# Performance work log

Measured on AMD Instinct MI355X. Metric: run time of the kernel, lower is better.

Reference implementation:

```python
import jax, jax.numpy as jnp
import numpy as np

TOP_K = 2

def setup_inputs() -> dict:
    key = jax.random.key(0)
    k0, k1, k2, k3 = jax.random.split(key, 4)
    B, T, D, F, E = 2, 2048, 1024, 4096, 8
    x = jax.random.normal(k0, (B, T, D), dtype=jnp.float32)
    Wr = jax.random.normal(k1, (E, D), dtype=jnp.float32) * 0.02   # router weight [out=E, in=D]
    W1 = jax.random.normal(k2, (E, F, D), dtype=jnp.float32) * 0.02  # per-expert up-proj [out=F, in=D]
    W2 = jax.random.normal(k3, (E, D, F), dtype=jnp.float32) * 0.02  # per-expert down-proj [out=D, in=F]
    return {"x": x, "Wr": Wr, "W1": W1, "W2": W2}

def reference(x, Wr, W1, W2):
    B, T, D = x.shape
    E = Wr.shape[0]
    N = B * T
    xf = x.reshape(N, D)
    # Router in fp32 on the un-cast activations (as in the torch module).
    logits = xf @ Wr.T                                   # [N, E]
    probs = jax.nn.softmax(logits, axis=-1)
    topk_w, topk_idx = jax.lax.top_k(probs, TOP_K)       # [N, K]
    topk_w = topk_w / jnp.sum(topk_w, axis=-1, keepdims=True)
    # Combine weights scattered into a dense [N, E] dispatch/combine matrix
    # (top_k indices are distinct, so .set is exact).
    combine = jnp.zeros((N, E), dtype=jnp.float32)
    combine = combine.at[jnp.arange(N)[:, None], topk_idx].set(topk_w)
    # Expert FFN runs in bf16 (comm_dtype in the original all-to-all pipeline).
    xb = xf.astype(jnp.bfloat16)
    h = jax.nn.gelu(jnp.einsum('nd,efd->enf', xb, W1.astype(jnp.bfloat16)),
                    approximate=False)                   # [E, N, F]
    yo = jnp.einsum('enf,edf->end', h, W2.astype(jnp.bfloat16))  # [E, N, D]
    # Weighted combine: bf16 expert outputs * fp32 gate weights -> fp32 (torch promotion).
    out = jnp.einsum('end,ne->nd', yo.astype(jnp.float32), combine)
    return out.reshape(B, T, D)
```

## Files before the change

kernel.cpp:

```cpp
#include <hip/hip_runtime.h>
#include <hip/hip_bf16.h>

typedef __attribute__((ext_vector_type(8))) __bf16 bf16x8;
typedef __attribute__((ext_vector_type(4))) float floatx4;

constexpr int N_TOK = 4096;
constexpr int DDIM  = 1024;
constexpr int FDIM  = 4096;
constexpr int NEXP  = 8;
constexpr int NSLOT = 2 * N_TOK;
constexpr int BM_T  = 256;
constexpr int MAXT  = NSLOT / BM_T + NEXP - 1;
constexpr int KSPLIT = 2;

static __device__ __forceinline__ unsigned short f2bf(float f) {
    union { __hip_bfloat16 h; unsigned short u; } v;
    v.h = __float2bfloat16(f);
    return v.u;
}

static __device__ __forceinline__ void gl2lds16(const unsigned short* g, unsigned short* l) {
    __builtin_amdgcn_global_load_lds(
        (__attribute__((address_space(1))) void*)g,
        (__attribute__((address_space(3))) void*)l,
        16, 0, 0);
}

__global__ void castW_kernel(const float* __restrict__ W1, const float* __restrict__ W2,
                             unsigned short* __restrict__ w1b, unsigned short* __restrict__ w2b,
                             int* __restrict__ counts) {
    constexpr int HALF = NEXP * FDIM * DDIM / 4;
    int i = blockIdx.x * 256 + threadIdx.x;
    const float* s; unsigned short* d; int j;
    if (i < HALF) { s = W1; d = w1b; j = i; }
    else          { s = W2; d = w2b; j = i - HALF; }
    float4 v = *(const float4*)(s + (size_t)j * 4);
    ushort4 o;
    o.x = f2bf(v.x); o.y = f2bf(v.y); o.z = f2bf(v.z); o.w = f2bf(v.w);
    *(ushort4*)(d + (size_t)j * 4) = o;
    if (blockIdx.x == 0 && threadIdx.x < NEXP) counts[threadIdx.x] = 0;
}

__global__ void router_kernel(const float* __restrict__ x, const float* __restrict__ Wr,
                              unsigned short* __restrict__ xb,
                              int* __restrict__ te, float* __restrict__ tw,
                              int* __restrict__ counts) {
    __shared__ float wr[NEXP * DDIM];
    const int tid = threadIdx.x;
    for (int i = tid; i < NEXP * DDIM; i += 256) wr[i] = Wr[i];
    __syncthreads();
    const int wave = tid >> 6, lane = tid & 63;
    const int t = blockIdx.x * 4 + wave;

    float xr[16];
    const float* xp = x + (size_t)t * DDIM;
    #pragma unroll
    for (int i = 0; i < 16; i++) xr[i] = xp[lane + 64 * i];

    unsigned short* xbp = xb + (size_t)t * DDIM;
    #pragma unroll
    for (int i = 0; i < 16; i++) xbp[lane + 64 * i] = f2bf(xr[i]);

    float logit[NEXP];
    #pragma unroll
    for (int e = 0; e < NEXP; e++) {
        float s = 0.f;
        #pragma unroll
        for (int i = 0; i < 16; i++) s += xr[i] * wr[e * DDIM + lane + 64 * i];
        #pragma unroll
        for (int off = 32; off > 0; off >>= 1) s += __shfl_xor(s, off, 64);
        logit[e] = s;
    }
    if (lane == 0) {
        int i0 = 0; float l0 = logit[0];
        #pragma unroll
        for (int e = 1; e < NEXP; e++) if (logit[e] > l0) { l0 = logit[e]; i0 = e; }
        int i1 = -1; float l1 = -3.0e38f;
        #pragma unroll
        for (int e = 0; e < NEXP; e++) if (e != i0 && logit[e] > l1) { l1 = logit[e]; i1 = e; }
        float p1 = expf(l1 - l0);
        float w0 = 1.f / (1.f + p1);
        float w1 = p1 * w0;
        te[t * 2] = i0; te[t * 2 + 1] = i1;
        tw[t * 2] = w0; tw[t * 2 + 1] = w1;
        atomicAdd(&counts[i0], 1);
        atomicAdd(&counts[i1], 1);
    }
}

__global__ void scan_scatter_kernel(const int* __restrict__ counts,
                                    const int* __restrict__ te, const float* __restrict__ tw,
                                    int* __restrict__ offsets, int* __restrict__ tile_em,
                                    int* __restrict__ ntile,
                                    int* __restrict__ rowid, float* __restrict__ gate,
                                    int* __restrict__ tok2slot) {
    __shared__ int soff[NEXP];
    __shared__ int scur[NEXP];
    const int tid = threadIdx.x;
    if (tid == 0) {
        int acc = 0, nt = 0;
        for (int e = 0; e < NEXP; e++) {
            offsets[e] = acc; soff[e] = acc;
            for (int m0 = 0; m0 < counts[e]; m0 += BM_T)
                tile_em[nt++] = (e << 16) | (m0 >> 8);
            acc += counts[e];
        }
        offsets[NEXP] = acc;
        ntile[0] = nt;
        for (int i = nt; i < MAXT; i++) tile_em[i] = 0;
    }
    if (tid < NEXP) scur[tid] = 0;
    __syncthreads();
    for (int t = tid; t < N_TOK; t += 256) {
        #pragma unroll
        for (int k = 0; k < 2; k++) {
            int e = te[t * 2 + k];
            int pos = atomicAdd(&scur[e], 1);
            int slot = soff[e] + pos;
            rowid[slot] = t;
            gate[slot] = tw[t * 2 + k];
            tok2slot[t * 2 + k] = slot;
        }
    }
}

template <bool UP>
__global__ __launch_bounds__(512)
void ffn_gemm(const unsigned short* __restrict__ A,
              const unsigned short* __restrict__ Wb,
              unsigned short* __restrict__ Hout,
              float* __restrict__ Y,
              const int* __restrict__ rowid,
              const float* __restrict__ gate,
              const int* __restrict__ offsets,
              const int* __restrict__ tile_em,
              const int* __restrict__ ntile) {
    constexpr int BM = 256;
    constexpr int BN = UP ? 256 : 128;
    constexpr int BK = 64;
    constexpr int NOUT = UP ? FDIM : DDIM;
    constexpr int KDIM = UP ? DDIM : FDIM;
    constexpr int NN   = NOUT / BN;
    constexpr int KLEN = UP ? DDIM : (FDIM / KSPLIT);
    constexpr int KT   = KLEN / BK;
    constexpr int WN_W = UP ? 4 : 2;
    constexpr int MREP = UP ? 8 : 4;
    constexpr int NREP = 4;
    constexpr int AINST = BM / 64;
    constexpr int BINST = BN / 64;
    constexpr int ASTRIDE = BM * BK;
    constexpr int BSTRIDE = BN * BK;

    const int nwg = NN * MAXT * (UP ? 1 : KSPLIT);
    const int orig = blockIdx.x;
    const int xcd = orig & 7, idx = orig >> 3;
    const int q = nwg >> 3, r = nwg & 7;
    const int id = (xcd < r ? xcd * (q + 1) : r * (q + 1) + (xcd - r) * q) + idx;

    const int n0 = (id % NN) * BN;
    const int bt = (id / NN) % MAXT;
    const int ks = UP ? 0 : (id / (NN * MAXT));
    if (bt >= ntile[0]) return;
    const int em = tile_em[bt];
    const int e  = em >> 16;
    const int m0 = (em & 0xffff) << 8;
    const int seg = offsets[e];
    const int cnt = offsets[e + 1] - seg;
    const int kbase = ks * KLEN;

    __shared__ __align__(16) unsigned short As[2 * ASTRIDE];
    __shared__ __align__(16) unsigned short Bs[2 * BSTRIDE];

    const int tid  = threadIdx.x;
    const int lane = tid & 63;
    const int wave = tid >> 6;
    const int lrow = lane >> 3;
    const int scol = ((lane & 7) ^ lrow) * 8;

    const unsigned short* ag[AINST];
    #pragma unroll
    for (int j = 0; j < AINST; j++) {
        int arow = wave * (BM / 8) + j * 8 + lrow;
        int slot = seg + m0 + arow;
        if (slot >= NSLOT) slot = NSLOT - 1;
        if (UP) { int t = rowid[slot]; ag[j] = A + (size_t)t * DDIM + kbase + scol; }
        else    { ag[j] = A + (size_t)slot * FDIM + kbase + scol; }
    }
    const unsigned short* bg[BINST];
    #pragma unroll
    for (int j = 0; j < BINST; j++) {
        int brow = wave * (BN / 8) + j * 8 + lrow;
        bg[j] = Wb + ((size_t)e * NOUT + n0 + brow) * KDIM + kbase + scol;
    }
    unsigned short* asl[AINST];
    unsigned short* bsl[BINST];
    #pragma unroll
    for (int j = 0; j < AINST; j++)
        asl[j] = &As[(wave * (BM / 8) + j * 8) * BK] + lane * 8;
    #pragma unroll
    for (int j = 0; j < BINST; j++)
        bsl[j] = &Bs[(wave * (BN / 8) + j * 8) * BK] + lane * 8;

    auto stage = [&](int b) {
        #pragma unroll
        for (int j = 0; j < AINST; j++) { gl2lds16(ag[j], asl[j] + b * ASTRIDE); ag[j] += BK; }
        #pragma unroll
        for (int j = 0; j < BINST; j++) { gl2lds16(bg[j], bsl[j] + b * BSTRIDE); bg[j] += BK; }
    };

    const int frow = lane & 15;
    const int quad = lane >> 4;
    const int wm = (wave / WN_W) * (MREP * 16);
    const int wn = (wave % WN_W) * 64;
    const int sxor = (frow & 7) << 3;

    floatx4 acc[MREP][NREP];
    #pragma unroll
    for (int i = 0; i < MREP; i++)
        #pragma unroll
        for (int j = 0; j < NREP; j++)
            acc[i][j] = (floatx4){0.f, 0.f, 0.f, 0.f};

    stage(0);
    __syncthreads();
    for (int kt = 0; kt < KT; kt++) {
        if (kt + 1 < KT) stage((kt + 1) & 1);
        const unsigned short* Ab = &As[(kt & 1) * ASTRIDE];
        const unsigned short* Bb = &Bs[(kt & 1) * BSTRIDE];
        #pragma unroll
        for (int h = 0; h < 2; h++) {
            const int cs = (h * 32 + quad * 8) ^ sxor;
            bf16x8 av[MREP], bv[NREP];
            #pragma unroll
            for (int i = 0; i < MREP; i++)
                av[i] = *(const bf16x8*)&Ab[(wm + i * 16 + frow) * BK + cs];
            #pragma unroll
            for (int j = 0; j < NREP; j++)
                bv[j] = *(const bf16x8*)&Bb[(wn + j * 16 + frow) * BK + cs];
            #pragma unroll
            for (int i = 0; i < MREP; i++)
                #pragma unroll
                for (int j = 0; j < NREP; j++)
                    acc[i][j] = __builtin_amdgcn_mfma_f32_16x16x32_bf16(av[i], bv[j], acc[i][j], 0, 0, 0);
        }
        __syncthreads();
    }

    #pragma unroll
    for (int mt = 0; mt < MREP; mt++) {
        #pragma unroll
        for (int rr = 0; rr < 4; rr++) {
            int mloc = m0 + wm + mt * 16 + quad * 4 + rr;
            if (mloc >= cnt) continue;
            int slot = seg + mloc;
            if (UP) {
                #pragma unroll
                for (int nt = 0; nt < NREP; nt++) {
                    int n = n0 + wn + nt * 16 + frow;
                    float v = acc[mt][nt][rr];
                    float g = 0.5f * v * (1.0f + erff(v * 0.70710678118654752f));
                    Hout[(size_t)slot * FDIM + n] = f2bf(g);
                }
            } else {
                float gw = gate[slot];
                #pragma unroll
                for (int nt = 0; nt < NREP; nt++) {
                    int n = n0 + wn + nt * 16 + frow;
                    Y[((size_t)ks * NSLOT + slot) * DDIM + n] = gw * acc[mt][nt][rr];
                }
            }
        }
    }
}

__global__ void combine_kernel(const float* __restrict__ Y, const int* __restrict__ tok2slot,
                               float* __restrict__ out) {
    int idx = blockIdx.x * 256 + threadIdx.x;
    int t = idx >> 8;
    int c = (idx & 255) * 4;
    int s0 = tok2slot[t * 2], s1 = tok2slot[t * 2 + 1];
    float4 r = make_float4(0.f, 0.f, 0.f, 0.f);
    #pragma unroll
    for (int ks = 0; ks < KSPLIT; ks++) {
        float4 a = *(const float4*)(Y + ((size_t)ks * NSLOT + s0) * DDIM + c);
        float4 b = *(const float4*)(Y + ((size_t)ks * NSLOT + s1) * DDIM + c);
        r.x += a.x + b.x; r.y += a.y + b.y; r.z += a.z + b.z; r.w += a.w + b.w;
    }
    *(float4*)(out + (size_t)t * DDIM + c) = r;
}

extern "C" void kernel_launch(void* const* d_in, const int* in_sizes, int n_in,
                              void* d_out, int out_size, void* d_ws, size_t ws_size,
                              hipStream_t stream) {
    const float* x  = (const float*)d_in[0];
    const float* Wr = (const float*)d_in[1];
    const float* W1 = (const float*)d_in[2];
    const float* W2 = (const float*)d_in[3];
    float* out = (float*)d_out;

    char* ws = (char*)d_ws;
    size_t off = 0;
    auto alloc = [&](size_t bytes) -> char* {
        char* p = ws + off;
        off = (off + bytes + 255) & ~(size_t)255;
        return p;
    };
    unsigned short* xb   = (unsigned short*)alloc((size_t)N_TOK * DDIM * 2);
    unsigned short* H    = (unsigned short*)alloc((size_t)NSLOT * FDIM * 2);
    float* Yb      = (float*)alloc((size_t)KSPLIT * NSLOT * DDIM * 4);
    int*   rowid   = (int*)alloc(NSLOT * 4);
    float* gatew   = (float*)alloc(NSLOT * 4);
    int*   te      = (int*)alloc(NSLOT * 4);
    float* tw      = (float*)alloc(NSLOT * 4);
    int*   t2s     = (int*)alloc(NSLOT * 4);
    int*   counts  = (int*)alloc(64);
    int*   offsets = (int*)alloc(64);
    int*   tile_em = (int*)alloc(MAXT * 4);
    int*   ntile   = (int*)alloc(64);
    unsigned short* w1b = (unsigned short*)alloc((size_t)NEXP * FDIM * DDIM * 2);
    unsigned short* w2b = (unsigned short*)alloc((size_t)NEXP * DDIM * FDIM * 2);
    (void)ws_size;

    constexpr int GRID_UP = (FDIM / 256) * MAXT;
    constexpr int GRID_DN = (DDIM / 128) * MAXT * KSPLIT;

    castW_kernel<<<2 * NEXP * FDIM * DDIM / 4 / 256, 256, 0, stream>>>(W1, W2, w1b, w2b, counts);
    router_kernel<<<N_TOK / 4, 256, 0, stream>>>(x, Wr, xb, te, tw, counts);
    scan_scatter_kernel<<<1, 256, 0, stream>>>(counts, te, tw, offsets, tile_em, ntile,
                                               rowid, gatew, t2s);
    ffn_gemm<true ><<<GRID_UP, 512, 0, stream>>>(xb, w1b, H, Yb, rowid, gatew,
                                                 offsets, tile_em, ntile);
    ffn_gemm<false><<<GRID_DN, 512, 0, stream>>>(H, w2b, H, Yb, rowid, gatew,
                                                 offsets, tile_em, ntile);
    combine_kernel<<<N_TOK, 256, 0, stream>>>(Yb, t2s, out);
}
```

Before: 762.2 us.

## Shrink GEMM tiles to BK=32, BN=128 with 4 blocks/CU occupancy

Re-tiles both expert GEMMs to a uniform 256x128x32 block with 4x4 MFMA repeats per wave and a new 4-chunk LDS swizzle. The kernel also requests 4 resident blocks per CU through launch bounds. Smaller K steps and LDS footprint are meant to raise occupancy and hide latency. In exchange the up-projection grid doubles, each MFMA pass does less work between barriers, and A tiles get reloaded more often.

```diff
diff --git a/kernel.cpp b/kernel.cpp
--- a/kernel.cpp
+++ b/kernel.cpp
@@ -125,7 +125,7 @@
 }
 
 template <bool UP>
-__global__ __launch_bounds__(512)
+__global__ __launch_bounds__(512, 4)
 void ffn_gemm(const unsigned short* __restrict__ A,
               const unsigned short* __restrict__ Wb,
               unsigned short* __restrict__ Hout,
@@ -135,27 +135,21 @@
               const int* __restrict__ offsets,
               const int* __restrict__ tile_em,
               const int* __restrict__ ntile) {
-    constexpr int BM = 256;
-    constexpr int BN = UP ? 256 : 128;
-    constexpr int BK = 64;
+    constexpr int BM = 256, BN = 128, BK = 32;
     constexpr int NOUT = UP ? FDIM : DDIM;
     constexpr int KDIM = UP ? DDIM : FDIM;
     constexpr int NN   = NOUT / BN;
     constexpr int KLEN = UP ? DDIM : (FDIM / KSPLIT);
     constexpr int KT   = KLEN / BK;
-    constexpr int WN_W = UP ? 4 : 2;
-    constexpr int MREP = UP ? 8 : 4;
-    constexpr int NREP = 4;
-    constexpr int AINST = BM / 64;
-    constexpr int BINST = BN / 64;
+    constexpr int MREP = 4, NREP = 4;
     constexpr int ASTRIDE = BM * BK;
     constexpr int BSTRIDE = BN * BK;
 
     const int nwg = NN * MAXT * (UP ? 1 : KSPLIT);
     const int orig = blockIdx.x;
     const int xcd = orig & 7, idx = orig >> 3;
-    const int q = nwg >> 3, r = nwg & 7;
-    const int id = (xcd < r ? xcd * (q + 1) : r * (q + 1) + (xcd - r) * q) + idx;
+    const int qq = nwg >> 3, rr8 = nwg & 7;
+    const int id = (xcd < rr8 ? xcd * (qq + 1) : rr8 * (qq + 1) + (xcd - rr8) * qq) + idx;
 
     const int n0 = (id % NN) * BN;
     const int bt = (id / NN) % MAXT;
@@ -174,45 +168,39 @@
     const int tid  = threadIdx.x;
     const int lane = tid & 63;
     const int wave = tid >> 6;
-    const int lrow = lane >> 3;
-    const int scol = ((lane & 7) ^ lrow) * 8;
-
-    const unsigned short* ag[AINST];
-    #pragma unroll
-    for (int j = 0; j < AINST; j++) {
-        int arow = wave * (BM / 8) + j * 8 + lrow;
+    const int lrow = lane >> 2;
+    const int chunk = lane & 3;
+    const int scol = (chunk ^ (lrow & 3)) * 8;
+
+    const unsigned short* ag[2];
+    #pragma unroll
+    for (int j = 0; j < 2; j++) {
+        int arow = wave * 32 + j * 16 + lrow;
         int slot = seg + m0 + arow;
         if (slot >= NSLOT) slot = NSLOT - 1;
         if (UP) { int t = rowid[slot]; ag[j] = A + (size_t)t * DDIM + kbase + scol; }
         else    { ag[j] = A + (size_t)slot * FDIM + kbase + scol; }
     }
-    const unsigned short* bg[BINST];
-    #pragma unroll
-    for (int j = 0; j < BINST; j++) {
-        int brow = wave * (BN / 8) + j * 8 + lrow;
-        bg[j] = Wb + ((size_t)e * NOUT + n0 + brow) * KDIM + kbase + scol;
-    }
-    unsigned short* asl[AINST];
-    unsigned short* bsl[BINST];
-    #pragma unroll
-    for (int j = 0; j < AINST; j++)
-        asl[j] = &As[(wave * (BM / 8) + j * 8) * BK] + lane * 8;
-    #pragma unroll
-    for (int j = 0; j < BINST; j++)
-        bsl[j] = &Bs[(wave * (BN / 8) + j * 8) * BK] + lane * 8;
+    const unsigned short* bg0 =
+        Wb + ((size_t)e * NOUT + n0 + wave * 16 + lrow) * KDIM + kbase + scol;
+
+    unsigned short* asl[2];
+    #pragma unroll
+    for (int j = 0; j < 2; j++)
+        asl[j] = &As[(wave * 32 + j * 16) * BK] + lane * 8;
+    unsigned short* bsl0 = &Bs[(wave * 16) * BK] + lane * 8;
 
     auto stage = [&](int b) {
-        #pragma unroll
-        for (int j = 0; j < AINST; j++) { gl2lds16(ag[j], asl[j] + b * ASTRIDE); ag[j] += BK; }
-        #pragma unroll
-        for (int j = 0; j < BINST; j++) { gl2lds16(bg[j], bsl[j] + b * BSTRIDE); bg[j] += BK; }
+        gl2lds16(ag[0], asl[0] + b * ASTRIDE); ag[0] += BK;
+        gl2lds16(ag[1], asl[1] + b * ASTRIDE); ag[1] += BK;
+        gl2lds16(bg0,   bsl0   + b * BSTRIDE); bg0   += BK;
     };
 
     const int frow = lane & 15;
     const int quad = lane >> 4;
-    const int wm = (wave / WN_W) * (MREP * 16);
-    const int wn = (wave % WN_W) * 64;
-    const int sxor = (frow & 7) << 3;
+    const int wm = (wave >> 1) * 64;
+    const int wn = (wave & 1) * 64;
+    const int cs = ((quad ^ (frow & 3)) * 8);
 
     floatx4 acc[MREP][NREP];
     #pragma unroll
@@ -227,37 +215,33 @@
         if (kt + 1 < KT) stage((kt + 1) & 1);
         const unsigned short* Ab = &As[(kt & 1) * ASTRIDE];
         const unsigned short* Bb = &Bs[(kt & 1) * BSTRIDE];
-        #pragma unroll
-        for (int h = 0; h < 2; h++) {
-            const int cs = (h * 32 + quad * 8) ^ sxor;
-            bf16x8 av[MREP], bv[NREP];
-            #pragma unroll
-            for (int i = 0; i < MREP; i++)
-                av[i] = *(const bf16x8*)&Ab[(wm + i * 16 + frow) * BK + cs];
+        bf16x8 av[MREP], bv[NREP];
+        #pragma unroll
+        for (int i = 0; i < MREP; i++)
+            av[i] = *(const bf16x8*)&Ab[(wm + i * 16 + frow) * BK + cs];
+        #pragma unroll
+        for (int j = 0; j < NREP; j++)
+            bv[j] = *(const bf16x8*)&Bb[(wn + j * 16 + frow) * BK + cs];
+        #pragma unroll
+        for (int i = 0; i < MREP; i++)
             #pragma unroll
             for (int j = 0; j < NREP; j++)
-                bv[j] = *(const bf16x8*)&Bb[(wn + j * 16 + frow) * BK + cs];
-            #pragma unroll
-            for (int i = 0; i < MREP; i++)
-                #pragma unroll
-                for (int j = 0; j < NREP; j++)
-                    acc[i][j] = __builtin_amdgcn_mfma_f32_16x16x32_bf16(av[i], bv[j], acc[i][j], 0, 0, 0);
-        }
+                acc[i][j] = __builtin_amdgcn_mfma_f32_16x16x32_bf16(av[i], bv[j], acc[i][j], 0, 0, 0);
         __syncthreads();
     }
 
     #pragma unroll
     for (int mt = 0; mt < MREP; mt++) {
         #pragma unroll
-        for (int rr = 0; rr < 4; rr++) {
-            int mloc = m0 + wm + mt * 16 + quad * 4 + rr;
+        for (int rg = 0; rg < 4; rg++) {
+            int mloc = m0 + wm + mt * 16 + quad * 4 + rg;
             if (mloc >= cnt) continue;
             int slot = seg + mloc;
             if (UP) {
                 #pragma unroll
                 for (int nt = 0; nt < NREP; nt++) {
                     int n = n0 + wn + nt * 16 + frow;
-                    float v = acc[mt][nt][rr];
+                    float v = acc[mt][nt][rg];
                     float g = 0.5f * v * (1.0f + erff(v * 0.70710678118654752f));
                     Hout[(size_t)slot * FDIM + n] = f2bf(g);
                 }
@@ -266,7 +250,7 @@
                 #pragma unroll
                 for (int nt = 0; nt < NREP; nt++) {
                     int n = n0 + wn + nt * 16 + frow;
-                    Y[((size_t)ks * NSLOT + slot) * DDIM + n] = gw * acc[mt][nt][rr];
+                    Y[((size_t)ks * NSLOT + slot) * DDIM + n] = gw * acc[mt][nt][rg];
                 }
             }
         }
@@ -321,7 +305,7 @@
     unsigned short* w2b = (unsigned short*)alloc((size_t)NEXP * DDIM * FDIM * 2);
     (void)ws_size;
 
-    constexpr int GRID_UP = (FDIM / 256) * MAXT;
+    constexpr int GRID_UP = (FDIM / 128) * MAXT;
     constexpr int GRID_DN = (DDIM / 128) * MAXT * KSPLIT;
 
     castW_kernel<<<2 * NEXP * FDIM * DDIM / 4 / 256, 256, 0, stream>>>(W1, W2, w1b, w2b, counts);
```

After: 683.9 us. 10.3% less time.
